# Kernel tuning notes

Hardware: AMD Instinct MI355X
Metric: run time of the kernel (lower is better)

## Reference

```python
import jax, jax.numpy as jnp
import numpy as np

B, L, E, H, DV, V = 256, 512, 200, 256, 30000, 50000
NEG_INF = -jnp.inf

def setup_inputs() -> dict:
    key = jax.random.key(0)
    ks = jax.random.split(key, 16)
    s = 0.05
    f = jnp.float32
    return {
        "input_id": jax.random.randint(ks[0], (B, 1), 0, V),
        "input_emb": jax.random.normal(ks[1], (B, 1, E), f),
        "encoder_outputs": jax.random.normal(ks[2], (B, L, H), f),
        "encoder_input_ids": jax.random.randint(ks[3], (B, L), 0, V),
        "hidden": jax.random.normal(ks[4], (B, 1, H), f),
        "attention": jax.random.normal(ks[5], (B, 1, H), f),
        # GRU (PyTorch layout): W_ih (3H, 2H+E), W_hh (3H, H), gate order r,z,n
        "W_ih": jax.random.normal(ks[6], (3 * H, 2 * H + E), f) * s,
        "W_hh": jax.random.normal(ks[7], (3 * H, H), f) * s,
        "b_ih": jnp.zeros((3 * H,), f),
        "b_hh": jnp.zeros((3 * H,), f),
        "W_attn": jax.random.normal(ks[8], (H, H), f) * s,
        "b_attn": jnp.zeros((H,), f),
        "W_comb": jax.random.normal(ks[9], (H, 2 * H), f) * s,
        "b_comb": jnp.zeros((H,), f),
        "W_gen": jax.random.normal(ks[10], (DV, H), f) * s,
        "b_gen": jnp.zeros((DV,), f),
        "W_copy": jax.random.normal(ks[11], (H, H), f) * s,
        "b_copy": jnp.zeros((H,), f),
    }


def reference(input_id, input_emb, encoder_outputs, encoder_input_ids, hidden,
              attention, W_ih, W_hh, b_ih, b_hh, W_attn, b_attn, W_comb,
              b_comb, W_gen, b_gen, W_copy, b_copy):
    b, l = encoder_input_ids.shape
    # selective read: rou = normalized match mask (NaN guard -> 0)
    mask = (input_id == encoder_input_ids).astype(encoder_outputs.dtype)  # (b,l)
    msum = jnp.sum(mask, axis=1, keepdims=True)
    rou = jnp.where(msum > 0, mask / jnp.where(msum > 0, msum, 1.0), 0.0)
    selective_read = jnp.einsum('bl,blh->bh', rou, encoder_outputs)  # (b,h)

    # GRU single step (dropout is identity at inference)
    x = jnp.concatenate([input_emb[:, 0], attention[:, 0], selective_read], axis=-1)
    h_prev = hidden[:, 0]  # (b,h)
    gx = x @ W_ih.T + b_ih          # (b,3h)
    gh = h_prev @ W_hh.T + b_hh     # (b,3h)
    xr, xz, xn = jnp.split(gx, 3, axis=-1)
    hr, hz, hn = jnp.split(gh, 3, axis=-1)
    r = jax.nn.sigmoid(xr + hr)
    z = jax.nn.sigmoid(xz + hz)
    n = jnp.tanh(xn + r * hn)
    h = (1.0 - z) * n + z * h_prev  # (b,h) cur_hidden

    # attention
    q = h @ W_attn.T + b_attn
    attn_w = jax.nn.softmax(jnp.einsum('bh,blh->bl', q, encoder_outputs), axis=-1)
    attn_applied = jnp.einsum('bl,blh->bh', attn_w, encoder_outputs)
    cur_attention = jnp.tanh(
        jnp.concatenate([attn_applied, h], axis=-1) @ W_comb.T + b_comb)  # (b,h)

    # generate + copy scores, joint softmax
    generate_score = cur_attention @ W_gen.T + b_gen                     # (b,DV)
    copy_weights = jax.nn.sigmoid(encoder_outputs @ W_copy.T + b_copy)   # (b,l,h)
    copy_score = jnp.einsum('blh,bh->bl', copy_weights, cur_attention)   # (b,l)
    score = jax.nn.softmax(jnp.concatenate([generate_score, copy_score], axis=1), axis=1)
    gen_s, copy_s = score[:, :DV], score[:, DV:]

    # fused equivalent of the one-hot scatter/mix: direct scatter-add into vocab
    output = jnp.zeros((b, V), score.dtype)
    output = output.at[:, :DV].add(gen_s)
    output = output.at[jnp.arange(b)[:, None], encoder_input_ids].add(copy_s)

    pos = output > 0
    out = jnp.where(pos, jnp.log(jnp.where(pos, output, 1.0)), NEG_INF)
    return out, h[:, None, :], cur_attention[:, None, :]
```

## Files before the change

### kernel.cpp

```cpp
#include <hip/hip_runtime.h>
#include <cmath>

#define B_  256
#define L_  512
#define E_  200
#define H_  256
#define DV_ 30000
#define V_  50000
#define X_  712
#define G3_ 768

#define NEG_BIG -1.0e30f

typedef __attribute__((ext_vector_type(8))) _Float16 half8;
typedef __attribute__((ext_vector_type(4))) float   floatx4;

#define GLOAD16(gptr, lptr)                                                            \
    __builtin_amdgcn_global_load_lds(                                                  \
        (const __attribute__((address_space(1))) unsigned int*)(gptr),                 \
        (__attribute__((address_space(3))) unsigned int*)(lptr), 16, 0, 0)

__global__ void k_cast_wc(const float* __restrict__ Wc, _Float16* __restrict__ wcb) {
    int i = blockIdx.x * 256 + threadIdx.x;
    wcb[i] = (_Float16)Wc[i];
}

__global__ void k_selread(const int* __restrict__ input_id, const float* __restrict__ emb,
                          const float* __restrict__ attention, const float* __restrict__ hidden,
                          const float* __restrict__ enc, const int* __restrict__ enc_ids,
                          float* __restrict__ xT) {
    int b = blockIdx.x, t = threadIdx.x;
    __shared__ int cnt;
    __shared__ int list[L_];
    if (t == 0) cnt = 0;
    __syncthreads();
    int id = input_id[b];
    for (int l = t; l < L_; l += 256) {
        if (enc_ids[b * L_ + l] == id) { int p = atomicAdd(&cnt, 1); list[p] = l; }
    }
    __syncthreads();
    int n = cnt;
    float s = 0.f;
    for (int i = 0; i < n; i++) s += enc[(b * L_ + list[i]) * H_ + t];
    float sel = (n > 0) ? s / (float)n : 0.f;
    for (int k = t; k < E_; k += 256) xT[k * B_ + b] = emb[b * E_ + k];
    xT[(E_ + t) * B_ + b]       = attention[b * H_ + t];
    xT[(E_ + H_ + t) * B_ + b]  = sel;
    xT[(X_ + t) * B_ + b]       = hidden[b * H_ + t];
}

template<int K>
__global__ void __launch_bounds__(256) k_gru_one(const float* __restrict__ xTp, const float* __restrict__ W,
                                                 const float* __restrict__ bias, float* __restrict__ g) {
    __shared__ __align__(16) float Ws[8 * K];
    int t  = threadIdx.x;
    int j0 = blockIdx.x * 8;
    int bq = t & 63;
    int jh = t >> 6;
#pragma unroll
    for (int jj = 0; jj < 8; jj++) {
        const float4* src = (const float4*)(W + (size_t)(j0 + jj) * K);
        float4* dst = (float4*)(Ws + jj * K);
        for (int i = t; i < K / 4; i += 256) dst[i] = src[i];
    }
    __syncthreads();
    float acc0[4] = {0.f, 0.f, 0.f, 0.f};
    float acc1[4] = {0.f, 0.f, 0.f, 0.f};
    const float* w0 = Ws + (jh * 2 + 0) * K;
    const float* w1 = Ws + (jh * 2 + 1) * K;
#pragma unroll 2
    for (int k4 = 0; k4 < K / 4; k4++) {
        float4 wa = *(const float4*)(w0 + k4 * 4);
        float4 wb = *(const float4*)(w1 + k4 * 4);
        float wav[4] = {wa.x, wa.y, wa.z, wa.w};
        float wbv[4] = {wb.x, wb.y, wb.z, wb.w};
#pragma unroll
        for (int u = 0; u < 4; u++) {
            float4 xv = *(const float4*)(xTp + (size_t)(k4 * 4 + u) * B_ + bq * 4);
            acc0[0] += wav[u] * xv.x; acc0[1] += wav[u] * xv.y;
            acc0[2] += wav[u] * xv.z; acc0[3] += wav[u] * xv.w;
            acc1[0] += wbv[u] * xv.x; acc1[1] += wbv[u] * xv.y;
            acc1[2] += wbv[u] * xv.z; acc1[3] += wbv[u] * xv.w;
        }
    }
    int ja = j0 + jh * 2, jb = ja + 1;
    float ba = bias[ja], bb = bias[jb];
#pragma unroll
    for (int i = 0; i < 4; i++) {
        g[(size_t)(bq * 4 + i) * G3_ + ja] = acc0[i] + ba;
        g[(size_t)(bq * 4 + i) * G3_ + jb] = acc1[i] + bb;
    }
}

__global__ void k_gru_gates(const float* __restrict__ gx, const float* __restrict__ gh,
                            const float* __restrict__ hidden, float* __restrict__ hws,
                            float* __restrict__ hout) {
    int b = blockIdx.x, j = threadIdx.x;
    float xr = gx[b * G3_ + j], xz = gx[b * G3_ + 256 + j], xn = gx[b * G3_ + 512 + j];
    float hr = gh[b * G3_ + j], hz = gh[b * G3_ + 256 + j], hn = gh[b * G3_ + 512 + j];
    float r = 1.f / (1.f + expf(-(xr + hr)));
    float z = 1.f / (1.f + expf(-(xz + hz)));
    float n = tanhf(xn + r * hn);
    float hp = hidden[b * H_ + j];
    float h = (1.f - z) * n + z * hp;
    hws[b * H_ + j] = h;
    hout[b * H_ + j] = h;
}

__global__ void __launch_bounds__(1024) k_attn(const float* __restrict__ hws, const float* __restrict__ enc,
                       const float* __restrict__ W_attn, const float* __restrict__ b_attn,
                       const float* __restrict__ W_comb, const float* __restrict__ b_comb,
                       float* __restrict__ caws, _Float16* __restrict__ cab,
                       float* __restrict__ caout) {
    int b = blockIdx.x, t = threadIdx.x;
    int lane = t & 63, w = t >> 6;
    int jj = t & 255, ph = t >> 8;
    __shared__ float hs[H_], qs[H_], sc[L_], ap[H_];
    __shared__ float part[4][H_];
    __shared__ float red[20];
    if (t < 256) hs[t] = hws[b * H_ + t];
    __syncthreads();
    {
        const float4* wr = (const float4*)(W_attn + (size_t)jj * H_ + ph * 64);
        const float4* hp = (const float4*)(hs + ph * 64);
        float acc = 0.f;
#pragma unroll
        for (int k4 = 0; k4 < 16; k4++) {
            float4 wv = wr[k4]; float4 hv = hp[k4];
            acc += wv.x * hv.x + wv.y * hv.y + wv.z * hv.z + wv.w * hv.w;
        }
        part[ph][jj] = acc;
    }
    __syncthreads();
    if (t < 256) qs[t] = b_attn[t] + part[0][t] + part[1][t] + part[2][t] + part[3][t];
    __syncthreads();
    {
        float4 q4 = *(const float4*)&qs[lane * 4];
        size_t base = (size_t)b * L_ + w * 32;
        for (int i = 0; i < 32; i += 4) {
            float s[4];
#pragma unroll
            for (int u = 0; u < 4; u++) {
                float4 e = *(const float4*)(enc + (base + i + u) * H_ + lane * 4);
                s[u] = q4.x * e.x + q4.y * e.y + q4.z * e.z + q4.w * e.w;
            }
#pragma unroll
            for (int u = 0; u < 4; u++) {
#pragma unroll
                for (int o = 1; o < 64; o <<= 1) s[u] += __shfl_xor(s[u], o);
                if (lane == 0) sc[w * 32 + i + u] = s[u];
            }
        }
    }
    __syncthreads();
    float ev = 0.f;
    if (t < 512) {
        float m = sc[t];
#pragma unroll
        for (int o = 1; o < 64; o <<= 1) m = fmaxf(m, __shfl_xor(m, o));
        if (lane == 0) red[w] = m;
    }
    __syncthreads();
    if (t == 0) {
        float m = red[0];
        for (int i = 1; i < 8; i++) m = fmaxf(m, red[i]);
        red[16] = m;
    }
    __syncthreads();
    if (t < 512) {
        ev = __expf(sc[t] - red[16]);
        float s = ev;
#pragma unroll
        for (int o = 1; o < 64; o <<= 1) s += __shfl_xor(s, o);
        if (lane == 0) red[8 + w] = s;
    }
    __syncthreads();
    if (t == 0) {
        float s = red[8];
        for (int i = 1; i < 8; i++) s += red[8 + i];
        red[17] = 1.f / s;
    }
    __syncthreads();
    if (t < 512) sc[t] = ev * red[17];
    __syncthreads();
    {
        size_t base = (size_t)b * L_ + ph * 128;
        float a0 = 0.f, a1 = 0.f, a2 = 0.f, a3 = 0.f;
        for (int l = 0; l < 128; l += 4) {
            a0 += sc[ph * 128 + l + 0] * enc[(base + l + 0) * H_ + jj];
            a1 += sc[ph * 128 + l + 1] * enc[(base + l + 1) * H_ + jj];
            a2 += sc[ph * 128 + l + 2] * enc[(base + l + 2) * H_ + jj];
            a3 += sc[ph * 128 + l + 3] * enc[(base + l + 3) * H_ + jj];
        }
        part[ph][jj] = (a0 + a1) + (a2 + a3);
    }
    __syncthreads();
    if (t < 256) ap[t] = part[0][t] + part[1][t] + part[2][t] + part[3][t];
    __syncthreads();
    {
        const float4* wr = (const float4*)(W_comb + (size_t)jj * (2 * H_) + ph * 128);
        const float4* xp = (const float4*)(((ph & 2) ? hs : ap) + (ph & 1) * 128);
        float acc = 0.f;
#pragma unroll
        for (int k4 = 0; k4 < 32; k4++) {
            float4 wv = wr[k4]; float4 xv = xp[k4];
            acc += wv.x * xv.x + wv.y * xv.y + wv.z * xv.z + wv.w * xv.w;
        }
        part[ph][jj] = acc;
    }
    __syncthreads();
    if (t < 256) {
        float cav = tanhf(b_comb[t] + part[0][t] + part[1][t] + part[2][t] + part[3][t]);
        caws[b * H_ + t] = cav;
        cab[b * H_ + t]  = (_Float16)cav;
        caout[b * H_ + t] = cav;
    }
}

__global__ void __launch_bounds__(256, 2) k_gen_mfma(
        const _Float16* __restrict__ cab, const float* __restrict__ W_gen,
        const float* __restrict__ b_gen, float* __restrict__ out) {
    __shared__ __align__(16) _Float16 Ah[128 * 32];
    __shared__ __align__(16) float    Bf[128 * 32];
    int t = threadIdx.x, w = t >> 6, lane = t & 63;
    int n0 = blockIdx.x * 128, m0 = blockIdx.y * 128;
    int wm = (w >> 1) * 64, wn = (w & 1) * 64;
    int l15 = lane & 15, q = lane >> 4;
    floatx4 acc[4][4];
#pragma unroll
    for (int i = 0; i < 4; i++)
#pragma unroll
        for (int j = 0; j < 4; j++) acc[i][j] = (floatx4){0.f, 0.f, 0.f, 0.f};

    for (int kc = 0; kc < H_; kc += 32) {
#pragma unroll
        for (int i = 0; i < 2; i++) {
            int t2 = w * 2 + i;
            int row = t2 * 16 + (lane >> 2);
            const _Float16* g = cab + (size_t)(m0 + row) * H_ + kc + (lane & 3) * 8;
            GLOAD16(g, &Ah[t2 * 512]);
        }
#pragma unroll
        for (int i = 0; i < 4; i++) {
            int t2 = w * 4 + i;
            int row = t2 * 8 + (lane >> 3);
            int nn = n0 + row; nn = nn < DV_ ? nn : DV_ - 1;
            const float* g = W_gen + (size_t)nn * H_ + kc + (lane & 7) * 4;
            GLOAD16(g, &Bf[t2 * 256]);
        }
        __syncthreads();
        half8 a[4];
#pragma unroll
        for (int mi = 0; mi < 4; mi++) {
            int m = wm + mi * 16 + l15;
            a[mi] = *(const half8*)&Ah[m * 32 + q * 8];
        }
#pragma unroll
        for (int ni = 0; ni < 4; ni++) {
            int n = wn + ni * 16 + l15;
            const float4* bp = (const float4*)&Bf[n * 32 + q * 8];
            float4 f0 = bp[0], f1 = bp[1];
            half8 bf;
            bf[0] = (_Float16)f0.x; bf[1] = (_Float16)f0.y; bf[2] = (_Float16)f0.z; bf[3] = (_Float16)f0.w;
            bf[4] = (_Float16)f1.x; bf[5] = (_Float16)f1.y; bf[6] = (_Float16)f1.z; bf[7] = (_Float16)f1.w;
#pragma unroll
            for (int mi = 0; mi < 4; mi++)
                acc[mi][ni] = __builtin_amdgcn_mfma_f32_16x16x32_f16(a[mi], bf, acc[mi][ni], 0, 0, 0);
        }
        __syncthreads();
    }
#pragma unroll
    for (int ni = 0; ni < 4; ni++) {
        int col = n0 + wn + ni * 16 + l15;
        if (col < DV_) {
            float bg = b_gen[col];
#pragma unroll
            for (int mi = 0; mi < 4; mi++)
#pragma unroll
                for (int j = 0; j < 4; j++) {
                    int row = m0 + wm + mi * 16 + q * 4 + j;
                    out[(size_t)row * V_ + col] = acc[mi][ni][j] + bg;
                }
        }
    }
}

__global__ void __launch_bounds__(256, 2) k_copy_mfma(
        const float* __restrict__ enc, const _Float16* __restrict__ wcb,
        const float* __restrict__ b_copy, const float* __restrict__ caws,
        float* __restrict__ copy_s) {
    __shared__ __align__(16) float    Af[128 * 32];
    __shared__ __align__(16) _Float16 Bh[256 * 32];
    __shared__ float bcs[H_], cas[H_];
    int t = threadIdx.x, w = t >> 6, lane = t & 63;
    int R0 = blockIdx.x * 128;
    int b  = blockIdx.x >> 2;
    int l15 = lane & 15, q = lane >> 4;
    bcs[t] = b_copy[t];
    cas[t] = caws[b * H_ + t];
    floatx4 acc[2][16];
#pragma unroll
    for (int i = 0; i < 2; i++)
#pragma unroll
        for (int j = 0; j < 16; j++) acc[i][j] = (floatx4){0.f, 0.f, 0.f, 0.f};

    for (int kc = 0; kc < H_; kc += 32) {
#pragma unroll
        for (int i = 0; i < 4; i++) {
            int t2 = w * 4 + i;
            int row = t2 * 8 + (lane >> 3);
            const float* g = enc + (size_t)(R0 + row) * H_ + kc + (lane & 7) * 4;
            GLOAD16(g, &Af[t2 * 256]);
        }
#pragma unroll
        for (int i = 0; i < 4; i++) {
            int t2 = w * 4 + i;
            int row = t2 * 16 + (lane >> 2);
            const _Float16* g = wcb + row * H_ + kc + (lane & 3) * 8;
            GLOAD16(g, &Bh[t2 * 512]);
        }
        __syncthreads();
        half8 a[2];
#pragma unroll
        for (int mi = 0; mi < 2; mi++) {
            int m = w * 32 + mi * 16 + l15;
            const float4* apx = (const float4*)&Af[m * 32 + q * 8];
            float4 f0 = apx[0], f1 = apx[1];
            half8 h;
            h[0] = (_Float16)f0.x; h[1] = (_Float16)f0.y; h[2] = (_Float16)f0.z; h[3] = (_Float16)f0.w;
            h[4] = (_Float16)f1.x; h[5] = (_Float16)f1.y; h[6] = (_Float16)f1.z; h[7] = (_Float16)f1.w;
            a[mi] = h;
        }
#pragma unroll
        for (int ni = 0; ni < 16; ni++) {
            int n = ni * 16 + l15;
            half8 bf = *(const half8*)&Bh[n * 32 + q * 8];
            acc[0][ni] = __builtin_amdgcn_mfma_f32_16x16x32_f16(a[0], bf, acc[0][ni], 0, 0, 0);
            acc[1][ni] = __builtin_amdgcn_mfma_f32_16x16x32_f16(a[1], bf, acc[1][ni], 0, 0, 0);
        }
        __syncthreads();
    }
#pragma unroll
    for (int mi = 0; mi < 2; mi++) {
#pragma unroll
        for (int j = 0; j < 4; j++) {
            float p = 0.f;
#pragma unroll
            for (int ni = 0; ni < 16; ni++) {
                int col = ni * 16 + l15;
                float v = acc[mi][ni][j] + bcs[col];
                p += cas[col] / (1.f + __expf(-v));
            }
            p += __shfl_xor(p, 1);
            p += __shfl_xor(p, 2);
            p += __shfl_xor(p, 4);
            p += __shfl_xor(p, 8);
            if (l15 == 0) copy_s[R0 + w * 32 + mi * 16 + q * 4 + j] = p;
        }
    }
}

__global__ void __launch_bounds__(1024) k_stats(const float* __restrict__ out, const float* __restrict__ copy_s,
                        float* __restrict__ mrow, float* __restrict__ ldrow) {
    int b = blockIdx.x, t = threadIdx.x, lane = t & 63, w = t >> 6;
    __shared__ float rm[16], rs[16];
    const float* row = out + (size_t)b * V_;
    float m = -INFINITY, s = 0.f;
    for (int j = t; j < DV_; j += 1024) {
        float v = row[j];
        if (v > m) { s = s * __expf(m - v) + 1.f; m = v; }
        else       s += __expf(v - m);
    }
    if (t < 512) {
        float v = copy_s[b * L_ + t];
        if (v > m) { s = s * __expf(m - v) + 1.f; m = v; }
        else       s += __expf(v - m);
    }
#pragma unroll
    for (int o = 1; o < 64; o <<= 1) {
        float m2 = __shfl_xor(m, o), s2 = __shfl_xor(s, o);
        float mn = fmaxf(m, m2);
        s = s * __expf(m - mn) + s2 * __expf(m2 - mn);
        m = mn;
    }
    if (lane == 0) { rm[w] = m; rs[w] = s; }
    __syncthreads();
    if (t == 0) {
        float M = rm[0], S = rs[0];
        for (int i = 1; i < 16; i++) {
            float mn = fmaxf(M, rm[i]);
            S = S * __expf(M - mn) + rs[i] * __expf(rm[i] - mn);
            M = mn;
        }
        mrow[b] = M;
        ldrow[b] = __logf(S);
    }
}

__global__ void __launch_bounds__(1024) k_final(float* __restrict__ out, const float* __restrict__ mrow,
                        const float* __restrict__ ldrow) {
    int j = blockIdx.x * 1024 + threadIdx.x;
    int b = blockIdx.y;
    if (j >= V_) return;
    size_t idx = (size_t)b * V_ + j;
    float sh = mrow[b] + ldrow[b];
    out[idx] = (j < DV_) ? out[idx] - sh : NEG_BIG;
}

__global__ void k_scatter_log(float* __restrict__ out, const float* __restrict__ copy_s,
                              const int* __restrict__ enc_ids, const float* __restrict__ mrow,
                              const float* __restrict__ ldrow) {
    int l = blockIdx.x * 256 + threadIdx.x;
    int b = blockIdx.y;
    float p = __expf(copy_s[b * L_ + l] - mrow[b] - ldrow[b]);
    unsigned int* up = (unsigned int*)(out + (size_t)b * V_ + enc_ids[b * L_ + l]);
    unsigned int cur = *up;
    while (true) {
        float ov = __uint_as_float(cur);
        float pv = (ov < -1.0e29f) ? p : __expf(ov) + p;
        unsigned int prev = atomicCAS(up, cur, __float_as_uint(__logf(pv)));
        if (prev == cur) break;
        cur = prev;
    }
}

extern "C" void kernel_launch(void* const* d_in, const int* in_sizes, int n_in,
                              void* d_out, int out_size, void* d_ws, size_t ws_size,
                              hipStream_t stream) {
    const int*   input_id  = (const int*)  d_in[0];
    const float* input_emb = (const float*)d_in[1];
    const float* enc       = (const float*)d_in[2];
    const int*   enc_ids   = (const int*)  d_in[3];
    const float* hidden    = (const float*)d_in[4];
    const float* attention = (const float*)d_in[5];
    const float* W_ih      = (const float*)d_in[6];
    const float* W_hh      = (const float*)d_in[7];
    const float* b_ih      = (const float*)d_in[8];
    const float* b_hh      = (const float*)d_in[9];
    const float* W_attn    = (const float*)d_in[10];
    const float* b_attn    = (const float*)d_in[11];
    const float* W_comb    = (const float*)d_in[12];
    const float* b_comb    = (const float*)d_in[13];
    const float* W_gen     = (const float*)d_in[14];
    const float* b_gen     = (const float*)d_in[15];
    const float* W_copy    = (const float*)d_in[16];
    const float* b_copy    = (const float*)d_in[17];

    float* out = (float*)d_out;
    float* ws  = (float*)d_ws;
    float* xT   = ws;
    float* gx   = xT + 247808;
    float* gh   = gx + 196608;
    float* hws  = gh + 196608;
    float* caws = hws + 65536;
    float* cps  = caws + 65536;
    float* mrow = cps + 131072;
    float* ldrow = mrow + 256;
    _Float16* wcb = (_Float16*)(ldrow + 256);
    _Float16* cab = wcb + 65536;

    float* hout  = out + (size_t)B_ * V_;
    float* caout = hout + B_ * H_;

    k_cast_wc<<<256, 256, 0, stream>>>(W_copy, wcb);
    k_selread<<<256, 256, 0, stream>>>(input_id, input_emb, attention, hidden, enc, enc_ids, xT);
    k_gru_one<712><<<96, 256, 0, stream>>>(xT, W_ih, b_ih, gx);
    k_gru_one<256><<<96, 256, 0, stream>>>(xT + X_ * B_, W_hh, b_hh, gh);
    k_gru_gates<<<256, 256, 0, stream>>>(gx, gh, hidden, hws, hout);
    k_attn<<<256, 1024, 0, stream>>>(hws, enc, W_attn, b_attn, W_comb, b_comb, caws, cab, caout);
    k_gen_mfma<<<dim3((DV_ + 127) / 128, 2), 256, 0, stream>>>(cab, W_gen, b_gen, out);
    k_copy_mfma<<<(B_ * L_) / 128, 256, 0, stream>>>(enc, wcb, b_copy, caws, cps);
    k_stats<<<256, 1024, 0, stream>>>(out, cps, mrow, ldrow);
    dim3 gf((V_ + 1023) / 1024, B_);
    k_final<<<gf, 1024, 0, stream>>>(out, mrow, ldrow);
    dim3 gs(L_ / 256, B_);
    k_scatter_log<<<gs, 256, 0, stream>>>(out, cps, enc_ids, mrow, ldrow);
}
```

Before: 488.1 us.

## Fuse attention scores, softmax and weighted sum into single-pass online softmax

The attention kernel now computes each wave's scores, an online (running max) softmax and the weighted accumulation of encoder rows in one pass. It reuses the encoder values already held in registers instead of reading the encoder block a second time. The separate softmax reduction stages and their barriers are removed, and per-wave partial results are merged with max rescaling. This costs extra exp work per row and more registers and shared memory (part grows to 16x256).

```diff
diff --git a/kernel.cpp b/kernel.cpp
--- a/kernel.cpp
+++ b/kernel.cpp
@@ -115,9 +115,9 @@
     int b = blockIdx.x, t = threadIdx.x;
     int lane = t & 63, w = t >> 6;
     int jj = t & 255, ph = t >> 8;
-    __shared__ float hs[H_], qs[H_], sc[L_], ap[H_];
-    __shared__ float part[4][H_];
-    __shared__ float red[20];
+    __shared__ float hs[H_], qs[H_], ap[H_];
+    __shared__ float part[16][H_];
+    __shared__ float rm[16], rd[16];
     if (t < 256) hs[t] = hws[b * H_ + t];
     __syncthreads();
     {
@@ -137,65 +137,52 @@
     {
         float4 q4 = *(const float4*)&qs[lane * 4];
         size_t base = (size_t)b * L_ + w * 32;
-        for (int i = 0; i < 32; i += 4) {
-            float s[4];
-#pragma unroll
-            for (int u = 0; u < 4; u++) {
-                float4 e = *(const float4*)(enc + (base + i + u) * H_ + lane * 4);
-                s[u] = q4.x * e.x + q4.y * e.y + q4.z * e.z + q4.w * e.w;
+        float m = -INFINITY, d = 0.f;
+        float ax = 0.f, ay = 0.f, az = 0.f, aw = 0.f;
+        for (int i = 0; i < 32; i += 8) {
+            float4 e[8];
+            float s[8];
+#pragma unroll
+            for (int u = 0; u < 8; u++) {
+                e[u] = *(const float4*)(enc + (base + i + u) * H_ + lane * 4);
+                s[u] = q4.x * e[u].x + q4.y * e[u].y + q4.z * e[u].z + q4.w * e[u].w;
             }
 #pragma unroll
-            for (int u = 0; u < 4; u++) {
+            for (int u = 0; u < 8; u++) {
 #pragma unroll
                 for (int o = 1; o < 64; o <<= 1) s[u] += __shfl_xor(s[u], o);
-                if (lane == 0) sc[w * 32 + i + u] = s[u];
             }
-        }
-    }
-    __syncthreads();
-    float ev = 0.f;
-    if (t < 512) {
-        float m = sc[t];
-#pragma unroll
-        for (int o = 1; o < 64; o <<= 1) m = fmaxf(m, __shfl_xor(m, o));
-        if (lane == 0) red[w] = m;
-    }
-    __syncthreads();
-    if (t == 0) {
-        float m = red[0];
-        for (int i = 1; i < 8; i++) m = fmaxf(m, red[i]);
-        red[16] = m;
-    }
-    __syncthreads();
-    if (t < 512) {
-        ev = __expf(sc[t] - red[16]);
-        float s = ev;
-#pragma unroll
-        for (int o = 1; o < 64; o <<= 1) s += __shfl_xor(s, o);
-        if (lane == 0) red[8 + w] = s;
-    }
-    __syncthreads();
-    if (t == 0) {
-        float s = red[8];
-        for (int i = 1; i < 8; i++) s += red[8 + i];
-        red[17] = 1.f / s;
-    }
-    __syncthreads();
-    if (t < 512) sc[t] = ev * red[17];
-    __syncthreads();
-    {
-        size_t base = (size_t)b * L_ + ph * 128;
-        float a0 = 0.f, a1 = 0.f, a2 = 0.f, a3 = 0.f;
-        for (int l = 0; l < 128; l += 4) {
-            a0 += sc[ph * 128 + l + 0] * enc[(base + l + 0) * H_ + jj];
-            a1 += sc[ph * 128 + l + 1] * enc[(base + l + 1) * H_ + jj];
-            a2 += sc[ph * 128 + l + 2] * enc[(base + l + 2) * H_ + jj];
-            a3 += sc[ph * 128 + l + 3] * enc[(base + l + 3) * H_ + jj];
-        }
-        part[ph][jj] = (a0 + a1) + (a2 + a3);
-    }
-    __syncthreads();
-    if (t < 256) ap[t] = part[0][t] + part[1][t] + part[2][t] + part[3][t];
+#pragma unroll
+            for (int u = 0; u < 8; u++) {
+                float mn = fmaxf(m, s[u]);
+                float fm = __expf(m - mn);
+                float fs = __expf(s[u] - mn);
+                d  = d  * fm + fs;
+                ax = ax * fm + fs * e[u].x;
+                ay = ay * fm + fs * e[u].y;
+                az = az * fm + fs * e[u].z;
+                aw = aw * fm + fs * e[u].w;
+                m = mn;
+            }
+        }
+        float* pw = &part[w][lane * 4];
+        pw[0] = ax; pw[1] = ay; pw[2] = az; pw[3] = aw;
+        if (lane == 0) { rm[w] = m; rd[w] = d; }
+    }
+    __syncthreads();
+    if (t < 256) {
+        float M = rm[0];
+#pragma unroll
+        for (int i = 1; i < 16; i++) M = fmaxf(M, rm[i]);
+        float den = 0.f, num = 0.f;
+#pragma unroll
+        for (int i = 0; i < 16; i++) {
+            float f = __expf(rm[i] - M);
+            den += rd[i] * f;
+            num += part[i][t] * f;
+        }
+        ap[t] = num / den;
+    }
     __syncthreads();
     {
         const float4* wr = (const float4*)(W_comb + (size_t)jj * (2 * H_) + ph * 128);
```

New measurement: 488.1 us. Within noise of the previous version (-0.0%).
